# Optimization experiments

Measured on AMD Instinct MI355X. Metric: run time of the kernel, lower is better.

The kernel has to match this reference:

```python
import jax, jax.numpy as jnp
import numpy as np

N_NODES = 100000
F_DIM = 128
D_LAT = 64
N_EDGES = 1000000
H_DIM = 128


def setup_inputs() -> dict:
    key = jax.random.key(0)
    ks = jax.random.split(key, 10)
    rng = np.random.default_rng(0)
    # positive edges (random graph) and non-edge negative pairs (dedup vs edge set,
    # mirroring the membership check in the torch elbo loop)
    edges = rng.integers(0, N_NODES, size=(2, N_EDGES))
    edge_hash = edges[0].astype(np.int64) * N_NODES + edges[1]
    cand = rng.integers(0, N_NODES, size=(2, 2 * N_EDGES))
    cand_hash = cand[0].astype(np.int64) * N_NODES + cand[1]
    keep = ~np.isin(cand_hash, edge_hash)
    neg = cand[:, keep][:, :N_EDGES]
    r = lambda k, s, sc=1.0: jax.random.normal(k, s, jnp.float32) * sc
    return {
        "x": r(ks[0], (N_NODES, F_DIM)),
        "eps": r(ks[1], (N_NODES, D_LAT)),
        "W_mu": r(ks[2], (F_DIM, D_LAT), 0.05),
        "b_mu": jnp.zeros((D_LAT,), jnp.float32),
        "W_lv": r(ks[3], (F_DIM, D_LAT), 0.05),
        "b_lv": jnp.zeros((D_LAT,), jnp.float32),
        "W1": r(ks[4], (D_LAT, H_DIM), 0.1),
        "b1": jnp.zeros((H_DIM,), jnp.float32),
        "W2": r(ks[5], (H_DIM, 1), 0.1),
        "b2": jnp.zeros((1,), jnp.float32),
        "edge_index": jnp.asarray(edges, jnp.int64) if jax.config.jax_enable_x64 else jnp.asarray(edges, jnp.int32),
        "neg_index": jnp.asarray(neg, jnp.int64) if jax.config.jax_enable_x64 else jnp.asarray(neg, jnp.int32),
    }


def reference(x, eps, W_mu, b_mu, W_lv, b_lv, W1, b1, W2, b2, edge_index, neg_index):
    # encoder: per-node diagonal Gaussian q(z|x)
    mu = x @ W_mu + b_mu            # [N, D]
    logvar = x @ W_lv + b_lv        # [N, D]
    z = mu + eps * jnp.exp(0.5 * logvar)  # q.rsample()

    def pair_logits(idx):
        zu = z[idx[0]]              # [E, D] gather
        zv = z[idx[1]]
        h = jax.nn.relu((zu * zv) @ W1 + b1)  # [E, H]
        return (h @ W2 + b2)[:, 0]  # [E]

    # Bernoulli(logits).log_prob(1) = log_sigmoid(l); log(1 - sigmoid(l)) = log_sigmoid(-l)
    true_lp = jax.nn.log_sigmoid(pair_logits(edge_index))
    false_lp = jax.nn.log_sigmoid(-pair_logits(neg_index))
    recon = jnp.mean(jnp.concatenate([true_lp, false_lp]))

    # KL(q || N(0, I)) per node, mean over nodes
    kl = jnp.mean(0.5 * jnp.sum(jnp.square(mu) + jnp.exp(logvar) - 1.0 - logvar, axis=-1))
    return -(recon - kl)
```

## Files before the change

kernel.cpp:

```cpp
#include <hip/hip_runtime.h>
#include <math.h>

#define F_DIM 128
#define D_LAT 64
#define H_DIM 128

typedef __attribute__((ext_vector_type(8))) short bf16x8;
typedef __attribute__((ext_vector_type(4))) float f32x4;
typedef __attribute__((ext_vector_type(2))) float f32x2;
typedef __attribute__((ext_vector_type(2))) unsigned long long u64x2;

__device__ __forceinline__ unsigned short f2bf(float f) {
    unsigned int u = __builtin_bit_cast(unsigned int, f);
    return (unsigned short)((u + 0x8000u) >> 16);
}

#define GLDS16(gaddr, laddr)                                                        \
    __builtin_amdgcn_global_load_lds(                                               \
        (const __attribute__((address_space(1))) void*)(gaddr),                     \
        (__attribute__((address_space(3))) void*)(laddr), 16, 0, 0)

__device__ __forceinline__ long prod_fp8(unsigned long long qu, unsigned long long qv) {
    const unsigned int ul = (unsigned int)qu, uh = (unsigned int)(qu >> 32);
    const unsigned int vl = (unsigned int)qv, vh = (unsigned int)(qv >> 32);
    const f32x2 u01 = __builtin_amdgcn_cvt_pk_f32_fp8(ul, false);
    const f32x2 u23 = __builtin_amdgcn_cvt_pk_f32_fp8(ul, true);
    const f32x2 u45 = __builtin_amdgcn_cvt_pk_f32_fp8(uh, false);
    const f32x2 u67 = __builtin_amdgcn_cvt_pk_f32_fp8(uh, true);
    const f32x2 v01 = __builtin_amdgcn_cvt_pk_f32_fp8(vl, false);
    const f32x2 v23 = __builtin_amdgcn_cvt_pk_f32_fp8(vl, true);
    const f32x2 v45 = __builtin_amdgcn_cvt_pk_f32_fp8(vh, false);
    const f32x2 v67 = __builtin_amdgcn_cvt_pk_f32_fp8(vh, true);
    const f32x2 p01 = u01 * v01, p23 = u23 * v23;
    const f32x2 p45 = u45 * v45, p67 = u67 * v67;
    unsigned int r0 = __builtin_amdgcn_cvt_pk_fp8_f32(p01[0], p01[1], 0u, false);
    r0 = __builtin_amdgcn_cvt_pk_fp8_f32(p23[0], p23[1], r0, true);
    unsigned int r1 = __builtin_amdgcn_cvt_pk_fp8_f32(p45[0], p45[1], 0u, false);
    r1 = __builtin_amdgcn_cvt_pk_fp8_f32(p67[0], p67[1], r1, true);
    return (long)(((unsigned long long)r1 << 32) | r0);
}

__global__ __launch_bounds__(256) void enc_mfma_kernel(
    const float* __restrict__ x, const float* __restrict__ eps,
    const float* __restrict__ Wmu, const float* __restrict__ bmu,
    const float* __restrict__ Wlv, const float* __restrict__ blv,
    unsigned char* __restrict__ zb, float* __restrict__ accum, int nNodes)
{
    const int lane = threadIdx.x & 63;
    const int li   = lane & 15;
    const int gi   = lane >> 4;

    bf16x8 wf[8][4];
#pragma unroll
    for (int t = 0; t < 4; ++t)
#pragma unroll
        for (int s = 0; s < 4; ++s)
#pragma unroll
            for (int j = 0; j < 8; ++j) {
                const int k = s * 32 + gi * 8 + j;
                wf[t][s][j]     = (short)f2bf(Wmu[k * D_LAT + 16 * t + li]);
                wf[t + 4][s][j] = (short)f2bf(Wlv[k * D_LAT + 16 * t + li]);
            }
    float bmu4[4], blv4[4];
#pragma unroll
    for (int t = 0; t < 4; ++t) {
        bmu4[t] = bmu[16 * t + li];
        blv4[t] = blv[16 * t + li];
    }

    const int wid = (blockIdx.x * blockDim.x + threadIdx.x) >> 6;
    const int nw  = (gridDim.x * blockDim.x) >> 6;
    const int NB  = nNodes >> 4;

    float klacc = 0.f;
    for (int nb = wid; nb < NB; nb += nw) {
        const int nbase = nb << 4;
        const float* __restrict__ xrow = x + (size_t)(nbase + li) * F_DIM;

        bf16x8 af[4];
#pragma unroll
        for (int s = 0; s < 4; ++s) {
            const f32x4 v0 = *(const f32x4*)(xrow + s * 32 + gi * 8);
            const f32x4 v1 = *(const f32x4*)(xrow + s * 32 + gi * 8 + 4);
#pragma unroll
            for (int j = 0; j < 4; ++j) {
                af[s][j]     = (short)f2bf(v0[j]);
                af[s][j + 4] = (short)f2bf(v1[j]);
            }
        }

        f32x4 acc[8];
#pragma unroll
        for (int t = 0; t < 4; ++t) {
            acc[t]     = (f32x4){bmu4[t], bmu4[t], bmu4[t], bmu4[t]};
            acc[t + 4] = (f32x4){blv4[t], blv4[t], blv4[t], blv4[t]};
        }
#pragma unroll
        for (int t = 0; t < 8; ++t)
#pragma unroll
            for (int s = 0; s < 4; ++s)
                acc[t] = __builtin_amdgcn_mfma_f32_16x16x32_bf16(af[s], wf[t][s], acc[t], 0, 0, 0);

#pragma unroll
        for (int r = 0; r < 4; ++r) {
            const int row = nbase + gi * 4 + r;
#pragma unroll
            for (int t = 0; t < 4; ++t) {
                const float mu  = acc[t][r];
                const float lv  = acc[t + 4][r];
                const float e05 = __expf(0.5f * lv);
                klacc += mu * mu + e05 * e05 - 1.0f - lv;
                const float zv = fmaf(eps[(size_t)row * D_LAT + 16 * t + li], e05, mu);
                zb[(size_t)row * D_LAT + 16 * t + li] =
                    (unsigned char)(__builtin_amdgcn_cvt_pk_fp8_f32(zv, 0.f, 0u, false) & 0xffu);
            }
        }
    }
    for (int off = 32; off; off >>= 1) klacc += __shfl_xor(klacc, off);
    if (lane == 0) atomicAdd(&accum[1], 0.5f * klacc);
}

__global__ __launch_bounds__(256) void edge_mfma_kernel(
    const unsigned char* __restrict__ zb,
    const int* __restrict__ eidx, const int* __restrict__ nidx,
    const float* __restrict__ W1, const float* __restrict__ b1,
    const float* __restrict__ W2, const float* __restrict__ b2,
    float* __restrict__ accum, int E)
{
    __shared__ unsigned char sh[4][2][2][1024];
    __shared__ long w1s[8][2][64];
    __shared__ float bw[2][H_DIM];

    const int lane = threadIdx.x & 63;
    const int li   = lane & 15;
    const int gi   = lane >> 4;
    const int w    = threadIdx.x >> 6;

    if (threadIdx.x < H_DIM) {
        bw[0][threadIdx.x] = b1[threadIdx.x];
        bw[1][threadIdx.x] = W2[threadIdx.x];
    }
#pragma unroll
    for (int k = 0; k < 2; ++k) {
        const int t = 2 * w + k;
#pragma unroll
        for (int s = 0; s < 2; ++s) {
            float f[8];
#pragma unroll
            for (int j = 0; j < 8; ++j)
                f[j] = W1[(gi * 16 + s * 8 + j) * H_DIM + 16 * t + li];
            unsigned int r0 = __builtin_amdgcn_cvt_pk_fp8_f32(f[0], f[1], 0u, false);
            r0 = __builtin_amdgcn_cvt_pk_fp8_f32(f[2], f[3], r0, true);
            unsigned int r1 = __builtin_amdgcn_cvt_pk_fp8_f32(f[4], f[5], 0u, false);
            r1 = __builtin_amdgcn_cvt_pk_fp8_f32(f[6], f[7], r1, true);
            w1s[t][s][lane] = (long)(((unsigned long long)r1 << 32) | r0);
        }
    }
    __syncthreads();

    const float b2v = b2[0];

    const int wid = (blockIdx.x * blockDim.x + threadIdx.x) >> 6;
    const int nw  = (gridDim.x * blockDim.x) >> 6;
    const int NBpos = E >> 4;
    const int NBH   = NBpos << 1;

    float lp = 0.f;

    auto load_idx = [&](int hb, int& u, int& v) {
        const int h = (hb < NBH) ? hb : (NBH - 1);
        const int* __restrict__ ia = (h < NBpos) ? eidx : nidx;
        const int m = ((h < NBpos) ? h : h - NBpos) << 4;
        u = ia[m + li]; v = ia[E + m + li];
    };
    auto stage = [&](int slot, int u, int v) {
        GLDS16(zb + (size_t)u * D_LAT + (gi << 4), &sh[w][slot][0][0]);
        GLDS16(zb + (size_t)v * D_LAT + (gi << 4), &sh[w][slot][1][0]);
    };

    int iu, iv;
    load_idx(wid, iu, iv);
    stage(0, iu, iv);
    load_idx(wid + nw, iu, iv);
    stage(1, iu, iv);
    load_idx(wid + 2 * nw, iu, iv);

    int slot = 0;
    for (int hb = wid; hb < NBH; hb += nw, slot ^= 1) {
        asm volatile("s_waitcnt vmcnt(4)" ::: "memory");
        const unsigned char* base = &sh[w][slot][0][0];
        const u64x2 qu = *(const u64x2*)(base + (lane << 4));
        const u64x2 qv = *(const u64x2*)(base + 1024 + (lane << 4));
        asm volatile("s_waitcnt lgkmcnt(0)" ::: "memory");

        int ju, jv;
        load_idx(hb + 3 * nw, ju, jv);
        stage(slot, iu, iv);
        iu = ju; iv = jv;

        const long pa0 = prod_fp8(qu[0], qv[0]);
        const long pa1 = prod_fp8(qu[1], qv[1]);

        float t0 = 0.f, t1 = 0.f, t2 = 0.f, t3 = 0.f;
#pragma unroll
        for (int t = 0; t < 8; ++t) {
            const float bb = bw[0][16 * t + li];
            f32x4 acc = (f32x4){bb, bb, bb, bb};
            acc = __builtin_amdgcn_mfma_f32_16x16x32_fp8_fp8(pa0, w1s[t][0][lane], acc, 0, 0, 0);
            acc = __builtin_amdgcn_mfma_f32_16x16x32_fp8_fp8(pa1, w1s[t][1][lane], acc, 0, 0, 0);
            const float w2v = bw[1][16 * t + li];
            t0 += fmaxf(acc[0], 0.f) * w2v;
            t1 += fmaxf(acc[1], 0.f) * w2v;
            t2 += fmaxf(acc[2], 0.f) * w2v;
            t3 += fmaxf(acc[3], 0.f) * w2v;
        }
#pragma unroll
        for (int off = 1; off < 16; off <<= 1) {
            t0 += __shfl_xor(t0, off);
            t1 += __shfl_xor(t1, off);
            t2 += __shfl_xor(t2, off);
            t3 += __shfl_xor(t3, off);
        }
        const float sg = (hb < NBpos) ? 1.f : -1.f;
        const float l0 = sg * (t0 + b2v), l1 = sg * (t1 + b2v);
        const float l2 = sg * (t2 + b2v), l3 = sg * (t3 + b2v);
        lp += fminf(l0, 0.f) - __logf(1.f + __expf(-fabsf(l0)));
        lp += fminf(l1, 0.f) - __logf(1.f + __expf(-fabsf(l1)));
        lp += fminf(l2, 0.f) - __logf(1.f + __expf(-fabsf(l2)));
        lp += fminf(l3, 0.f) - __logf(1.f + __expf(-fabsf(l3)));
    }

    for (int off = 32; off; off >>= 1) lp += __shfl_xor(lp, off);
    if (lane == 0) atomicAdd(&accum[0], lp * 0.0625f);
}

__global__ void fin_kernel(const float* __restrict__ accum, float* __restrict__ out,
                           int nNodes, int E)
{
    const float recon = accum[0] / (float)(2 * E);
    const float kl    = accum[1] / (float)nNodes;
    out[0] = kl - recon;
}

extern "C" void kernel_launch(void* const* d_in, const int* in_sizes, int n_in,
                              void* d_out, int out_size, void* d_ws, size_t ws_size,
                              hipStream_t stream)
{
    const float* x    = (const float*)d_in[0];
    const float* eps  = (const float*)d_in[1];
    const float* Wmu  = (const float*)d_in[2];
    const float* bmu  = (const float*)d_in[3];
    const float* Wlv  = (const float*)d_in[4];
    const float* blv  = (const float*)d_in[5];
    const float* W1   = (const float*)d_in[6];
    const float* b1   = (const float*)d_in[7];
    const float* W2   = (const float*)d_in[8];
    const float* b2   = (const float*)d_in[9];
    const int*   eidx = (const int*)d_in[10];
    const int*   nidx = (const int*)d_in[11];

    const int nNodes = in_sizes[1] / D_LAT;
    const int E      = in_sizes[10] / 2;

    float* accum      = (float*)d_ws;
    unsigned char* zb = (unsigned char*)((char*)d_ws + 256);

    hipMemsetAsync(accum, 0, 256, stream);
    enc_mfma_kernel<<<512, 256, 0, stream>>>(x, eps, Wmu, bmu, Wlv, blv, zb, accum, nNodes);
    edge_mfma_kernel<<<1536, 256, 0, stream>>>(zb, eidx, nidx, W1, b1, W2, b2, accum, E);
    fin_kernel<<<1, 1, 0, stream>>>(accum, (float*)d_out, nNodes, E);
}
```

Before: 176.0 us.

## Quantize latent z to FP4 and gather 32-byte rows in edge kernel

Adds a repack kernel that converts the fp8 latent table into packed 4-bit e2m1-style codes, which halves each node row to 32 bytes. The edge kernel now processes 32 pairs per wave-iteration, gathering half-size rows, and expands the nibbles back to fp8 through byte permutes before the MFMA MLP. This is meant to cut gather bandwidth in the memory-bound edge phase. The cost is an extra kernel pass over z and a large loss of precision in the latent values, which may push the loss result outside tolerance.

```diff
diff --git a/kernel.cpp b/kernel.cpp
--- a/kernel.cpp
+++ b/kernel.cpp
@@ -8,7 +8,6 @@
 typedef __attribute__((ext_vector_type(8))) short bf16x8;
 typedef __attribute__((ext_vector_type(4))) float f32x4;
 typedef __attribute__((ext_vector_type(2))) float f32x2;
-typedef __attribute__((ext_vector_type(2))) unsigned long long u64x2;
 
 __device__ __forceinline__ unsigned short f2bf(float f) {
     unsigned int u = __builtin_bit_cast(unsigned int, f);
@@ -40,6 +39,19 @@
     return (long)(((unsigned long long)r1 << 32) | r0);
 }
 
+__device__ __forceinline__ unsigned int nib4_to_fp8(unsigned int sel4) {
+    const unsigned int m = sel4 & 0x07070707u;
+    const unsigned int s = (sel4 & 0x08080808u) << 4;
+    return __builtin_amdgcn_perm(0x4C484440u, 0x3C383000u, m) | s;
+}
+__device__ __forceinline__ unsigned long long fp4x8_to_fp8(unsigned int x) {
+    const unsigned int e = x & 0x0F0F0F0Fu;
+    const unsigned int o = (x >> 4) & 0x0F0F0F0Fu;
+    const unsigned int sl = __builtin_amdgcn_perm(e, o, 0x01050004u);
+    const unsigned int sh = __builtin_amdgcn_perm(e, o, 0x03070206u);
+    return ((unsigned long long)nib4_to_fp8(sh) << 32) | nib4_to_fp8(sl);
+}
+
 __global__ __launch_bounds__(256) void enc_mfma_kernel(
     const float* __restrict__ x, const float* __restrict__ eps,
     const float* __restrict__ Wmu, const float* __restrict__ bmu,
@@ -120,8 +132,34 @@
     if (lane == 0) atomicAdd(&accum[1], 0.5f * klacc);
 }
 
+__global__ __launch_bounds__(256) void repack_fp4_kernel(
+    const unsigned char* __restrict__ zb, unsigned int* __restrict__ zb4, int n8)
+{
+    const int stride = gridDim.x * blockDim.x;
+    for (int i = blockIdx.x * blockDim.x + threadIdx.x; i < n8; i += stride) {
+        const unsigned long long q = *(const unsigned long long*)(zb + (size_t)i * 8);
+        float f[8];
+        f32x2 d;
+        d = __builtin_amdgcn_cvt_pk_f32_fp8((unsigned int)q, false);  f[0] = d[0]; f[1] = d[1];
+        d = __builtin_amdgcn_cvt_pk_f32_fp8((unsigned int)q, true);   f[2] = d[0]; f[3] = d[1];
+        d = __builtin_amdgcn_cvt_pk_f32_fp8((unsigned int)(q >> 32), false); f[4] = d[0]; f[5] = d[1];
+        d = __builtin_amdgcn_cvt_pk_f32_fp8((unsigned int)(q >> 32), true);  f[6] = d[0]; f[7] = d[1];
+        unsigned int out = 0;
+#pragma unroll
+        for (int k = 0; k < 8; ++k) {
+            const float a = fabsf(f[k]);
+            unsigned int n = (a < 0.25f) ? 0u : (a < 0.75f) ? 1u : (a < 1.25f) ? 2u :
+                             (a < 1.75f) ? 3u : (a < 2.5f)  ? 4u : (a < 3.5f)  ? 5u :
+                             (a < 5.0f)  ? 6u : 7u;
+            if (f[k] < 0.f) n |= 8u;
+            out |= n << (4 * k);
+        }
+        zb4[i] = out;
+    }
+}
+
 __global__ __launch_bounds__(256) void edge_mfma_kernel(
-    const unsigned char* __restrict__ zb,
+    const unsigned char* __restrict__ zb4,
     const int* __restrict__ eidx, const int* __restrict__ nidx,
     const float* __restrict__ W1, const float* __restrict__ b1,
     const float* __restrict__ W2, const float* __restrict__ b2,
@@ -162,20 +200,22 @@
 
     const int wid = (blockIdx.x * blockDim.x + threadIdx.x) >> 6;
     const int nw  = (gridDim.x * blockDim.x) >> 6;
-    const int NBpos = E >> 4;
+    const int NBpos = E >> 5;
     const int NBH   = NBpos << 1;
 
     float lp = 0.f;
+    const int myPair = lane >> 1;
+    const int chunk  = (lane & 1) << 4;
 
     auto load_idx = [&](int hb, int& u, int& v) {
         const int h = (hb < NBH) ? hb : (NBH - 1);
         const int* __restrict__ ia = (h < NBpos) ? eidx : nidx;
-        const int m = ((h < NBpos) ? h : h - NBpos) << 4;
-        u = ia[m + li]; v = ia[E + m + li];
+        const int m = ((h < NBpos) ? h : h - NBpos) << 5;
+        u = ia[m + myPair]; v = ia[E + m + myPair];
     };
     auto stage = [&](int slot, int u, int v) {
-        GLDS16(zb + (size_t)u * D_LAT + (gi << 4), &sh[w][slot][0][0]);
-        GLDS16(zb + (size_t)v * D_LAT + (gi << 4), &sh[w][slot][1][0]);
+        GLDS16(zb4 + (size_t)u * 32 + chunk, &sh[w][slot][0][0]);
+        GLDS16(zb4 + (size_t)v * 32 + chunk, &sh[w][slot][1][0]);
     };
 
     int iu, iv;
@@ -188,9 +228,13 @@
     int slot = 0;
     for (int hb = wid; hb < NBH; hb += nw, slot ^= 1) {
         asm volatile("s_waitcnt vmcnt(4)" ::: "memory");
-        const unsigned char* base = &sh[w][slot][0][0];
-        const u64x2 qu = *(const u64x2*)(base + (lane << 4));
-        const u64x2 qv = *(const u64x2*)(base + 1024 + (lane << 4));
+        const unsigned char* ubuf = &sh[w][slot][0][0];
+        const unsigned char* vbuf = &sh[w][slot][1][0];
+
+        const unsigned long long qu0 = *(const unsigned long long*)(ubuf + li * 32 + gi * 8);
+        const unsigned long long qv0 = *(const unsigned long long*)(vbuf + li * 32 + gi * 8);
+        const unsigned long long qu1 = *(const unsigned long long*)(ubuf + (16 + li) * 32 + gi * 8);
+        const unsigned long long qv1 = *(const unsigned long long*)(vbuf + (16 + li) * 32 + gi * 8);
         asm volatile("s_waitcnt lgkmcnt(0)" ::: "memory");
 
         int ju, jv;
@@ -198,36 +242,42 @@
         stage(slot, iu, iv);
         iu = ju; iv = jv;
 
-        const long pa0 = prod_fp8(qu[0], qv[0]);
-        const long pa1 = prod_fp8(qu[1], qv[1]);
-
-        float t0 = 0.f, t1 = 0.f, t2 = 0.f, t3 = 0.f;
-#pragma unroll
-        for (int t = 0; t < 8; ++t) {
-            const float bb = bw[0][16 * t + li];
-            f32x4 acc = (f32x4){bb, bb, bb, bb};
-            acc = __builtin_amdgcn_mfma_f32_16x16x32_fp8_fp8(pa0, w1s[t][0][lane], acc, 0, 0, 0);
-            acc = __builtin_amdgcn_mfma_f32_16x16x32_fp8_fp8(pa1, w1s[t][1][lane], acc, 0, 0, 0);
-            const float w2v = bw[1][16 * t + li];
-            t0 += fmaxf(acc[0], 0.f) * w2v;
-            t1 += fmaxf(acc[1], 0.f) * w2v;
-            t2 += fmaxf(acc[2], 0.f) * w2v;
-            t3 += fmaxf(acc[3], 0.f) * w2v;
-        }
-#pragma unroll
-        for (int off = 1; off < 16; off <<= 1) {
-            t0 += __shfl_xor(t0, off);
-            t1 += __shfl_xor(t1, off);
-            t2 += __shfl_xor(t2, off);
-            t3 += __shfl_xor(t3, off);
-        }
         const float sg = (hb < NBpos) ? 1.f : -1.f;
-        const float l0 = sg * (t0 + b2v), l1 = sg * (t1 + b2v);
-        const float l2 = sg * (t2 + b2v), l3 = sg * (t3 + b2v);
-        lp += fminf(l0, 0.f) - __logf(1.f + __expf(-fabsf(l0)));
-        lp += fminf(l1, 0.f) - __logf(1.f + __expf(-fabsf(l1)));
-        lp += fminf(l2, 0.f) - __logf(1.f + __expf(-fabsf(l2)));
-        lp += fminf(l3, 0.f) - __logf(1.f + __expf(-fabsf(l3)));
+#pragma unroll
+        for (int b = 0; b < 2; ++b) {
+            const unsigned long long qu = b ? qu1 : qu0;
+            const unsigned long long qv = b ? qv1 : qv0;
+            const long pa0 = prod_fp8(fp4x8_to_fp8((unsigned int)qu),
+                                      fp4x8_to_fp8((unsigned int)qv));
+            const long pa1 = prod_fp8(fp4x8_to_fp8((unsigned int)(qu >> 32)),
+                                      fp4x8_to_fp8((unsigned int)(qv >> 32)));
+            float t0 = 0.f, t1 = 0.f, t2 = 0.f, t3 = 0.f;
+#pragma unroll
+            for (int t = 0; t < 8; ++t) {
+                const float bb = bw[0][16 * t + li];
+                f32x4 acc = (f32x4){bb, bb, bb, bb};
+                acc = __builtin_amdgcn_mfma_f32_16x16x32_fp8_fp8(pa0, w1s[t][0][lane], acc, 0, 0, 0);
+                acc = __builtin_amdgcn_mfma_f32_16x16x32_fp8_fp8(pa1, w1s[t][1][lane], acc, 0, 0, 0);
+                const float w2v = bw[1][16 * t + li];
+                t0 += fmaxf(acc[0], 0.f) * w2v;
+                t1 += fmaxf(acc[1], 0.f) * w2v;
+                t2 += fmaxf(acc[2], 0.f) * w2v;
+                t3 += fmaxf(acc[3], 0.f) * w2v;
+            }
+#pragma unroll
+            for (int off = 1; off < 16; off <<= 1) {
+                t0 += __shfl_xor(t0, off);
+                t1 += __shfl_xor(t1, off);
+                t2 += __shfl_xor(t2, off);
+                t3 += __shfl_xor(t3, off);
+            }
+            const float l0 = sg * (t0 + b2v), l1 = sg * (t1 + b2v);
+            const float l2 = sg * (t2 + b2v), l3 = sg * (t3 + b2v);
+            lp += fminf(l0, 0.f) - __logf(1.f + __expf(-fabsf(l0)));
+            lp += fminf(l1, 0.f) - __logf(1.f + __expf(-fabsf(l1)));
+            lp += fminf(l2, 0.f) - __logf(1.f + __expf(-fabsf(l2)));
+            lp += fminf(l3, 0.f) - __logf(1.f + __expf(-fabsf(l3)));
+        }
     }
 
     for (int off = 32; off; off >>= 1) lp += __shfl_xor(lp, off);
@@ -262,11 +312,14 @@
     const int nNodes = in_sizes[1] / D_LAT;
     const int E      = in_sizes[10] / 2;
 
-    float* accum      = (float*)d_ws;
-    unsigned char* zb = (unsigned char*)((char*)d_ws + 256);
+    char* ws = (char*)d_ws;
+    float*         accum = (float*)ws;
+    unsigned char* zb    = (unsigned char*)(ws + 256);
+    unsigned char* zb4   = (unsigned char*)(ws + 6400512);
 
     hipMemsetAsync(accum, 0, 256, stream);
     enc_mfma_kernel<<<512, 256, 0, stream>>>(x, eps, Wmu, bmu, Wlv, blv, zb, accum, nNodes);
-    edge_mfma_kernel<<<1536, 256, 0, stream>>>(zb, eidx, nidx, W1, b1, W2, b2, accum, E);
+    repack_fp4_kernel<<<3125, 256, 0, stream>>>(zb, (unsigned int*)zb4, nNodes * 8);
+    edge_mfma_kernel<<<1536, 256, 0, stream>>>(zb4, eidx, nidx, W1, b1, W2, b2, accum, E);
     fin_kernel<<<1, 1, 0, stream>>>(accum, (float*)d_out, nNodes, E);
 }
```

Result: no change. 174.3 us (-1.0%).
